# Optimization experiments

Hardware: AMD Instinct MI355X
Metric: run time of the kernel (lower is better)

## Reference

```python
import jax, jax.numpy as jnp
import numpy as np

B, S, H = 2, 2048, 2048
NH, HD = 16, 128
I = 8192
EPS = float(np.finfo(np.float32).eps)  # torch RMSNorm default eps=None -> dtype eps


def rmsnorm(x, w):
    var = jnp.mean(jnp.square(x), axis=-1, keepdims=True)
    return x * jax.lax.rsqrt(var + EPS) * w


def setup_inputs() -> dict:
    key = jax.random.key(0)
    ks = jax.random.split(key, 8)
    s = 0.02
    return {
        "hidden_states": jax.random.normal(ks[0], (B, S, H), jnp.float32),
        "Wq": jax.random.normal(ks[1], (H, H), jnp.float32) * s,
        "Wk": jax.random.normal(ks[2], (H, H), jnp.float32) * s,
        "Wv": jax.random.normal(ks[3], (H, H), jnp.float32) * s,
        "Wo": jax.random.normal(ks[4], (H, H), jnp.float32) * s,
        "Wg": jax.random.normal(ks[5], (I, H), jnp.float32) * s,
        "Wu": jax.random.normal(ks[6], (I, H), jnp.float32) * s,
        "Wd": jax.random.normal(ks[7], (H, I), jnp.float32) * s,
        "g_in": jnp.ones((H,), jnp.float32),
        "g_post": jnp.ones((H,), jnp.float32),
    }


def reference(hidden_states, Wq, Wk, Wv, Wo, Wg, Wu, Wd, g_in, g_post):
    residual = hidden_states
    x = rmsnorm(hidden_states, g_in)
    # projections: nn.Linear does x @ W.T
    q = (x @ Wq.T).reshape(B, S, NH, HD).transpose(0, 2, 1, 3)  # [B,NH,S,HD]
    k = (x @ Wk.T).reshape(B, S, NH, HD).transpose(0, 2, 1, 3)
    v = (x @ Wv.T).reshape(B, S, NH, HD).transpose(0, 2, 1, 3)
    scores = jnp.einsum("bhqd,bhkd->bhqk", q, k) / jnp.sqrt(jnp.float32(HD))
    attn = jax.nn.softmax(scores, axis=-1)
    out = jnp.einsum("bhqk,bhkd->bhqd", attn, v)
    out = out.transpose(0, 2, 1, 3).reshape(B, S, H)
    hidden_states = residual + out @ Wo.T
    residual = hidden_states
    x = rmsnorm(hidden_states, g_post)
    mlp = (jax.nn.silu(x @ Wg.T) * (x @ Wu.T)) @ Wd.T
    return residual + mlp
```

## Files before the change

### kernel.cpp

```cpp
#include <hip/hip_runtime.h>

using u16 = unsigned short;
using u32 = unsigned int;

typedef __attribute__((ext_vector_type(8))) __bf16 bf16x8;
typedef __attribute__((ext_vector_type(4))) float f32x4;

__device__ __forceinline__ u16 f2bf(float f) {
  __bf16 h = (__bf16)f;
  return __builtin_bit_cast(u16, h);
}
__device__ __forceinline__ u32 pk2(float a, float b) {
  return (u32)f2bf(a) | ((u32)f2bf(b) << 16);
}
__device__ __forceinline__ float bf2f(u16 h) {
  return __uint_as_float(((u32)h) << 16);
}
__device__ __forceinline__ void gload16(const u16* g, u16* l) {
  __builtin_amdgcn_global_load_lds((const __attribute__((address_space(1))) void*)g,
                                   (__attribute__((address_space(3))) void*)l, 16, 0, 0);
}
__device__ __forceinline__ f32x4 mfma_bf16(bf16x8 a, bf16x8 b, f32x4 c) {
  return __builtin_amdgcn_mfma_f32_16x16x32_bf16(a, b, c, 0, 0, 0);
}

__global__ __launch_bounds__(256) void cvt_bf16(const float* __restrict__ in,
                                                u16* __restrict__ out, int n8) {
  int i = blockIdx.x * 256 + threadIdx.x;
  int stride = gridDim.x * 256;
  for (; i < n8; i += stride) {
    float4 a = ((const float4*)in)[(size_t)i * 2];
    float4 b = ((const float4*)in)[(size_t)i * 2 + 1];
    ((uint4*)out)[i] = make_uint4(pk2(a.x, a.y), pk2(a.z, a.w), pk2(b.x, b.y), pk2(b.z, b.w));
  }
}

__global__ __launch_bounds__(256) void rmsnorm_bf16(const float* __restrict__ x,
                                                    const float* __restrict__ g,
                                                    u16* __restrict__ o) {
  const int row = blockIdx.x;
  const int tid = threadIdx.x;
  const float4* xr = (const float4*)(x + (size_t)row * 2048);
  float4 a = xr[tid * 2], b = xr[tid * 2 + 1];
  float s = a.x * a.x + a.y * a.y + a.z * a.z + a.w * a.w +
            b.x * b.x + b.y * b.y + b.z * b.z + b.w * b.w;
#pragma unroll
  for (int off = 1; off < 64; off <<= 1) s += __shfl_xor(s, off);
  __shared__ float red[4];
  if ((tid & 63) == 0) red[tid >> 6] = s;
  __syncthreads();
  s = red[0] + red[1] + red[2] + red[3];
  const float r = rsqrtf(s * (1.0f / 2048.0f) + 1.1920929e-07f);
  const float4* gr = (const float4*)g;
  float4 ga = gr[tid * 2], gb = gr[tid * 2 + 1];
  ((uint4*)(o + (size_t)row * 2048))[tid] =
      make_uint4(pk2(a.x * r * ga.x, a.y * r * ga.y), pk2(a.z * r * ga.z, a.w * r * ga.w),
                 pk2(b.x * r * gb.x, b.y * r * gb.y), pk2(b.z * r * gb.z, b.w * r * gb.w));
}

template <int EPI>
__global__ __launch_bounds__(512, 2) void gemm4p(const u16* __restrict__ A,
                                                 const u16* __restrict__ B,
                                                 u16* Cb, float* Cf,
                                                 const float* __restrict__ Res,
                                                 int M, int N, int K, int lda) {
  alignas(16) __shared__ u16 lds[8 * 8192];
  const int tid = threadIdx.x;
  const int w = tid >> 6, lane = tid & 63;
  const int lo = lane & 15, hi = lane >> 4;
  const int nbm = M >> 8, nbx = N >> 8;
  const int RM = nbm >> 1, RN = nbx >> 2;
  const int xcd = blockIdx.x & 7, bidx = blockIdx.x >> 3;
  const int bm = ((xcd >> 2) * RM + bidx / RN) << 8;
  const int bn = ((xcd & 3) * RN + bidx % RN) << 8;
  const int wm = w >> 2, wn = w & 3;

  const int rw = (hi ^ ((lo >> 1) & 3)) * 8;
  const int arow0 = wm * 128 + lo, brow0 = wn * 64 + lo;

  const int srow = tid >> 2;
  const int scol = ((tid & 3) ^ ((tid >> 3) & 3)) * 8;
  const u16* Ab = A + (size_t)(bm + srow) * lda + scol;
  const u16* Bb = B + (size_t)(bn + srow) * K + scol;

  f32x4 acc[8][4] = {};
  bf16x8 af[4], bf[4];

#define SLOT(par, kh, op) ((((par) * 2 + (kh)) * 2 + (op)) * 8192)
#define STG(par, kh, op, kt)                                                   \
  {                                                                            \
    const u16* g_ = (op) ? Bb : Ab;                                            \
    const int ld_ = (op) ? K : lda;                                            \
    gload16(g_ + (kt) + (kh) * 32, &lds[SLOT(par, kh, op) + tid * 8]);         \
    gload16(g_ + (size_t)128 * ld_ + (kt) + (kh) * 32,                         \
            &lds[SLOT(par, kh, op) + 4096 + tid * 8]);                         \
  }
#define PHASE_OPEN()                                       \
  __builtin_amdgcn_s_barrier();                            \
  asm volatile("s_waitcnt lgkmcnt(0)" ::: "memory");       \
  __builtin_amdgcn_sched_barrier(0);
#define MFMA16(mb)                                                             \
  __builtin_amdgcn_s_setprio(1);                                               \
  _Pragma("unroll") for (int m_ = 0; m_ < 4; ++m_)                             \
      _Pragma("unroll") for (int n_ = 0; n_ < 4; ++n_)                         \
          acc[m_ + (mb)][n_] = mfma_bf16(af[m_], bf[n_], acc[m_ + (mb)][n_]);  \
  __builtin_amdgcn_s_setprio(0);

  STG(0, 0, 0, 0); STG(0, 0, 1, 0); STG(0, 1, 0, 0); STG(0, 1, 1, 0);
  asm volatile("s_waitcnt vmcnt(0)" ::: "memory");
  __builtin_amdgcn_s_barrier();

  const int NT = K >> 6;
  for (int t = 0; t < NT; ++t) {
    const int par = t & 1, np = par ^ 1;
    const int ktn = (t + 1) << 6;
    const bool pre = (t + 1 < NT);
    const u16* LA0 = &lds[SLOT(par, 0, 0)];
    const u16* LB0 = &lds[SLOT(par, 0, 1)];
    const u16* LA1 = &lds[SLOT(par, 1, 0)];
    const u16* LB1 = &lds[SLOT(par, 1, 1)];

#pragma unroll
    for (int n = 0; n < 4; ++n) bf[n] = *(const bf16x8*)(LB0 + (brow0 + n * 16) * 32 + rw);
#pragma unroll
    for (int m = 0; m < 4; ++m) af[m] = *(const bf16x8*)(LA0 + (arow0 + m * 16) * 32 + rw);
    if (pre) STG(np, 0, 0, ktn);
    PHASE_OPEN();
    MFMA16(0);
    __builtin_amdgcn_s_barrier();

#pragma unroll
    for (int m = 0; m < 4; ++m)
      af[m] = *(const bf16x8*)(LA0 + (arow0 + (m + 4) * 16) * 32 + rw);
    if (pre) STG(np, 0, 1, ktn);
    PHASE_OPEN();
    MFMA16(4);
    if (pre) { asm volatile("s_waitcnt vmcnt(4)" ::: "memory"); }
    else     { asm volatile("s_waitcnt vmcnt(0)" ::: "memory"); }
    __builtin_amdgcn_s_barrier();

#pragma unroll
    for (int n = 0; n < 4; ++n) bf[n] = *(const bf16x8*)(LB1 + (brow0 + n * 16) * 32 + rw);
#pragma unroll
    for (int m = 0; m < 4; ++m) af[m] = *(const bf16x8*)(LA1 + (arow0 + m * 16) * 32 + rw);
    if (pre) STG(np, 1, 0, ktn);
    PHASE_OPEN();
    MFMA16(0);
    __builtin_amdgcn_s_barrier();

#pragma unroll
    for (int m = 0; m < 4; ++m)
      af[m] = *(const bf16x8*)(LA1 + (arow0 + (m + 4) * 16) * 32 + rw);
    if (pre) STG(np, 1, 1, ktn);
    PHASE_OPEN();
    MFMA16(4);
    if (pre) { asm volatile("s_waitcnt vmcnt(4)" ::: "memory"); }
    __builtin_amdgcn_s_barrier();
  }
#undef SLOT
#undef STG
#undef PHASE_OPEN
#undef MFMA16

#pragma unroll
  for (int m = 0; m < 8; ++m) {
    const int gr = bm + wm * 128 + m * 16 + hi * 4;
#pragma unroll
    for (int n = 0; n < 4; ++n) {
      const int gc = bn + wn * 64 + n * 16 + lo;
#pragma unroll
      for (int r = 0; r < 4; ++r) {
        const size_t idx = (size_t)(gr + r) * N + gc;
        if constexpr (EPI == 1) {
          Cf[idx] = Res[idx] + acc[m][n][r];
        } else if constexpr (EPI == 2) {
          float g = bf2f(Cb[idx]);
          float s = g / (1.f + __expf(-g));
          Cb[idx] = f2bf(s * acc[m][n][r]);
        } else {
          Cb[idx] = f2bf(acc[m][n][r]);
        }
      }
    }
  }
}

template <int EPI>
__global__ __launch_bounds__(512, 1) void gemm3b(const u16* __restrict__ A,
                                                 const u16* __restrict__ B,
                                                 u16* Cb, float* Cf,
                                                 const float* __restrict__ Res,
                                                 int M, int N, int K, int lda) {
  constexpr int BUF = 24576;
  alignas(16) __shared__ u16 lds[3 * BUF];
  const int tid = threadIdx.x;
  const int w = tid >> 6, lane = tid & 63;
  const int lo = lane & 15, hi = lane >> 4;

  const int nbm = M >> 8, nbx = N >> 7;
  const int RM = nbm >> 1, RN = nbx >> 2;
  const int xcd = blockIdx.x & 7, idx = blockIdx.x >> 3;
  const int bm = ((xcd >> 2) * RM + idx / RN) << 8;
  const int bn = ((xcd & 3) * RN + idx % RN) << 7;

  const int wm = w >> 1, wn = w & 1;
  const int scol = ((tid & 7) ^ ((tid >> 3) & 7)) * 8;
  const u16* Ag = A + (size_t)(bm + (tid >> 3)) * lda + scol;
  const u16* Bg = B + (size_t)(bn + (tid >> 3)) * K + scol;

  f32x4 acc[4][4] = {};

#define STG(b, kt)                                                                    \
  {                                                                                   \
    _Pragma("unroll") for (int c = 0; c < 4; ++c)                                     \
        gload16(Ag + (size_t)(c * 64) * lda + (kt), &lds[(b)*BUF + c * 4096 + tid * 8]); \
    _Pragma("unroll") for (int c = 0; c < 2; ++c)                                     \
        gload16(Bg + (size_t)(c * 64) * K + (kt), &lds[(b)*BUF + 16384 + c * 4096 + tid * 8]); \
  }

  const int NT = K >> 6;
  STG(0, 0);
  STG(1, 64);

  int cur = 0;
  for (int T = 0; T < NT; ++T) {
    if (T + 1 < NT) {
      asm volatile("s_waitcnt vmcnt(6)" ::: "memory");
    } else {
      asm volatile("s_waitcnt vmcnt(0)" ::: "memory");
    }
    __builtin_amdgcn_s_barrier();
    __builtin_amdgcn_sched_barrier(0);

    const u16* LA = &lds[cur * BUF];
    const u16* LB = LA + 16384;
    bf16x8 af[4][2], bf[4][2];
#pragma unroll
    for (int ks = 0; ks < 2; ++ks) {
#pragma unroll
      for (int m = 0; m < 4; ++m)
        af[m][ks] = *(const bf16x8*)(LA + (wm * 64 + m * 16 + lo) * 64 +
                                     ((ks * 4 + hi) ^ (lo & 7)) * 8);
#pragma unroll
      for (int n = 0; n < 4; ++n)
        bf[n][ks] = *(const bf16x8*)(LB + (wn * 64 + n * 16 + lo) * 64 +
                                     ((ks * 4 + hi) ^ (lo & 7)) * 8);
    }
    if (T + 2 < NT) {
      const int nb = (cur + 2) % 3;
      STG(nb, (T + 2) << 6);
    }
    __builtin_amdgcn_s_setprio(1);
#pragma unroll
    for (int ks = 0; ks < 2; ++ks)
#pragma unroll
      for (int m = 0; m < 4; ++m)
#pragma unroll
        for (int n = 0; n < 4; ++n) acc[m][n] = mfma_bf16(af[m][ks], bf[n][ks], acc[m][n]);
    __builtin_amdgcn_s_setprio(0);
    cur = (cur + 1) % 3;
  }
#undef STG

#pragma unroll
  for (int m = 0; m < 4; ++m) {
    const int gr = bm + wm * 64 + m * 16 + hi * 4;
#pragma unroll
    for (int n = 0; n < 4; ++n) {
      const int gc = bn + wn * 64 + n * 16 + lo;
#pragma unroll
      for (int r = 0; r < 4; ++r) {
        const size_t idx2 = (size_t)(gr + r) * N + gc;
        if constexpr (EPI == 1) {
          Cf[idx2] = Res[idx2] + acc[m][n][r];
        } else if constexpr (EPI == 2) {
          float g = bf2f(Cb[idx2]);
          float s = g / (1.f + __expf(-g));
          Cb[idx2] = f2bf(s * acc[m][n][r]);
        } else {
          Cb[idx2] = f2bf(acc[m][n][r]);
        }
      }
    }
  }
}

template <int EPI>
__global__ __launch_bounds__(256) void gemm_bt(const u16* __restrict__ A,
                                               const float* __restrict__ B,
                                               u16* Cb, float* Cf, const float* Res,
                                               int M, int N, int K) {
  alignas(16) __shared__ u16 As[128 * 32];
  alignas(16) __shared__ u16 Bs[128 * 32];
  const int tid = threadIdx.x;
  const int w = tid >> 6, lane = tid & 63;
  const int lo = lane & 15, hi = lane >> 4;
  const int bm = blockIdx.y * 128, bn = blockIdx.x * 128;
  const int wr = (w >> 1) * 64, wc = (w & 1) * 64;
  f32x4 acc[4][4] = {};
  const int r0 = tid >> 2, kc0 = (tid & 3) * 8;
  const u16* a0 = A + (size_t)(bm + r0) * K + kc0;
  const u16* a1 = A + (size_t)(bm + 64 + r0) * K + kc0;
  const float* b0 = B + (size_t)(bn + r0) * K + kc0;
  const float* b1 = B + (size_t)(bn + 64 + r0) * K + kc0;
  u16* asd0 = &As[(size_t)tid * 8];
  u16* asd1 = &As[(size_t)(tid + 256) * 8];
  u16* bsd0 = &Bs[(size_t)tid * 8];
  u16* bsd1 = &Bs[(size_t)(tid + 256) * 8];
  for (int kt = 0; kt < K; kt += 32) {
    gload16(a0 + kt, asd0);
    gload16(a1 + kt, asd1);
    float4 x0 = *(const float4*)(b0 + kt);
    float4 x1 = *(const float4*)(b0 + kt + 4);
    float4 y0 = *(const float4*)(b1 + kt);
    float4 y1 = *(const float4*)(b1 + kt + 4);
    *(uint4*)bsd0 = make_uint4(pk2(x0.x, x0.y), pk2(x0.z, x0.w), pk2(x1.x, x1.y), pk2(x1.z, x1.w));
    *(uint4*)bsd1 = make_uint4(pk2(y0.x, y0.y), pk2(y0.z, y0.w), pk2(y1.x, y1.y), pk2(y1.z, y1.w));
    __syncthreads();
    bf16x8 af[4], bfr[4];
#pragma unroll
    for (int i = 0; i < 4; ++i) {
      af[i] = *(const bf16x8*)(&As[(wr + i * 16 + lo) * 32 + hi * 8]);
      bfr[i] = *(const bf16x8*)(&Bs[(wc + i * 16 + lo) * 32 + hi * 8]);
    }
#pragma unroll
    for (int i = 0; i < 4; ++i)
#pragma unroll
      for (int j = 0; j < 4; ++j) acc[i][j] = mfma_bf16(af[i], bfr[j], acc[i][j]);
    __syncthreads();
  }
#pragma unroll
  for (int i = 0; i < 4; ++i) {
    const int gr = bm + wr + i * 16 + hi * 4;
#pragma unroll
    for (int j = 0; j < 4; ++j) {
      const int gc = bn + wc + j * 16 + lo;
#pragma unroll
      for (int r = 0; r < 4; ++r) {
        const size_t idx = (size_t)(gr + r) * N + gc;
        if constexpr (EPI == 1) {
          Cf[idx] = Res[idx] + acc[i][j][r];
        } else if constexpr (EPI == 2) {
          float g = bf2f(Cb[idx]);
          float s = g / (1.f + __expf(-g));
          Cb[idx] = f2bf(s * acc[i][j][r]);
        } else {
          Cb[idx] = f2bf(acc[i][j][r]);
        }
      }
    }
  }
}

__global__ __launch_bounds__(256) void transpose_v(const u16* __restrict__ v,
                                                   u16* __restrict__ vt, int ldv) {
  __shared__ u16 t[32][33];
  const int bh = blockIdx.z, b = bh >> 4, h = bh & 15;
  const int s0 = blockIdx.x * 32, d0 = blockIdx.y * 32;
  const int tx = threadIdx.x, ty = threadIdx.y;
#pragma unroll
  for (int i = 0; i < 4; ++i)
    t[ty + i * 8][tx] = v[(size_t)(b * 2048 + s0 + ty + i * 8) * ldv + h * 128 + d0 + tx];
  __syncthreads();
#pragma unroll
  for (int i = 0; i < 4; ++i)
    vt[(size_t)(bh * 128 + d0 + ty + i * 8) * 2048 + s0 + tx] = t[tx][ty + i * 8];
}

__global__ __launch_bounds__(256) void attn_fwd2(const u16* __restrict__ q,
                                                 const u16* __restrict__ k,
                                                 const u16* __restrict__ vt,
                                                 u16* o, int ldq) {
  constexpr int S = 2048;
  alignas(16) __shared__ u16 Ks[2][64 * 128];
  alignas(16) __shared__ u16 Vs[2][128 * 64];
  alignas(16) __shared__ u16 plds[4][16 * 68];
  const int bh = blockIdx.y, b = bh >> 4, h = bh & 15;
  const int tid = threadIdx.x, w = tid >> 6, lane = tid & 63;
  const int lo = lane & 15, hi = lane >> 4;
  const int qr = blockIdx.x * 64 + w * 16;
  u16* pl = &plds[w][0];

  bf16x8 qf[4];
  const u16* qb = q + (size_t)(b * S + qr + lo) * ldq + h * 128 + hi * 8;
#pragma unroll
  for (int ks = 0; ks < 4; ++ks) qf[ks] = *(const bf16x8*)(qb + ks * 32);

  f32x4 oacc[8] = {};
  f32x4 lp = {0.f, 0.f, 0.f, 0.f};

  const u16* kb = k + (size_t)(b * S) * ldq + h * 128;
  const u16* vb = vt + (size_t)bh * 128 * S;

  const int kcs = ((((tid & 15) * 16) ^ (((tid >> 4) & 7) << 4)) >> 1);
  const int vcs = ((((tid & 7) * 16) ^ (((tid >> 3) & 7) << 4)) >> 1);
  const u16* kgs = kb + (size_t)(tid >> 4) * ldq + kcs;
  const u16* vgs = vb + (size_t)(tid >> 3) * S + vcs;

  int cur = 0;
#pragma unroll
  for (int c = 0; c < 4; ++c) gload16(kgs + (size_t)(c * 16) * ldq, &Ks[0][c * 2048 + tid * 8]);
#pragma unroll
  for (int c = 0; c < 4; ++c) gload16(vgs + (size_t)(c * 32) * S, &Vs[0][c * 2048 + tid * 8]);
  __syncthreads();

  const int swq = (lo & 7) << 4;
  constexpr float SCL = 0.12752956f;

  for (int kv = 0; kv < S; kv += 64) {
    if (kv + 64 < S) {
      const int nb = cur ^ 1;
#pragma unroll
      for (int c = 0; c < 4; ++c)
        gload16(kgs + (size_t)(kv + 64 + c * 16) * ldq, &Ks[nb][c * 2048 + tid * 8]);
#pragma unroll
      for (int c = 0; c < 4; ++c)
        gload16(vgs + (size_t)(c * 32) * S + kv + 64, &Vs[nb][c * 2048 + tid * 8]);
    }
    const u16* Kc = &Ks[cur][0];
    const u16* Vc = &Vs[cur][0];

    f32x4 sacc[4] = {};
    __builtin_amdgcn_s_setprio(1);
#pragma unroll
    for (int ks = 0; ks < 4; ++ks)
#pragma unroll
      for (int n = 0; n < 4; ++n) {
        bf16x8 kf = *(const bf16x8*)(Kc + (n * 16 + lo) * 128 + (((ks * 64 + hi * 16) ^ swq) >> 1));
        sacc[n] = mfma_bf16(qf[ks], kf, sacc[n]);
      }
    __builtin_amdgcn_s_setprio(0);

    f32x4 p[4];
#pragma unroll
    for (int n = 0; n < 4; ++n)
#pragma unroll
      for (int r = 0; r < 4; ++r) p[n][r] = exp2f(sacc[n][r] * SCL);
#pragma unroll
    for (int r = 0; r < 4; ++r)
      lp[r] += (p[0][r] + p[1][r]) + (p[2][r] + p[3][r]);

#pragma unroll
    for (int n = 0; n < 4; ++n)
#pragma unroll
      for (int r = 0; r < 4; ++r)
        pl[(hi * 4 + r) * 68 + n * 16 + lo] = f2bf(p[n][r]);
    asm volatile("s_waitcnt lgkmcnt(0)" ::: "memory");
    bf16x8 pf0 = *(const bf16x8*)(pl + lo * 68 + hi * 8);
    bf16x8 pf1 = *(const bf16x8*)(pl + lo * 68 + 32 + hi * 8);

    __builtin_amdgcn_s_setprio(1);
#pragma unroll
    for (int f = 0; f < 8; ++f) {
      const int row = f * 16 + lo;
      bf16x8 vf0 = *(const bf16x8*)(Vc + row * 64 + (((hi * 16) ^ swq) >> 1));
      bf16x8 vf1 = *(const bf16x8*)(Vc + row * 64 + (((64 + hi * 16) ^ swq) >> 1));
      oacc[f] = mfma_bf16(pf0, vf0, oacc[f]);
      oacc[f] = mfma_bf16(pf1, vf1, oacc[f]);
    }
    __builtin_amdgcn_s_setprio(0);

    __syncthreads();
    cur ^= 1;
  }

  float l[4];
#pragma unroll
  for (int r = 0; r < 4; ++r) l[r] = lp[r];
#pragma unroll
  for (int off = 1; off < 16; off <<= 1)
#pragma unroll
    for (int r = 0; r < 4; ++r) l[r] += __shfl_xor(l[r], off);

  u16* ob = o + (size_t)(b * S + qr) * ldq + h * 128;
#pragma unroll
  for (int f = 0; f < 8; ++f)
#pragma unroll
    for (int r = 0; r < 4; ++r)
      ob[(size_t)(hi * 4 + r) * ldq + f * 16 + lo] = f2bf(oacc[f][r] / l[r]);
}

extern "C" void kernel_launch(void* const* d_in, const int* in_sizes, int n_in,
                              void* d_out, int out_size, void* d_ws, size_t ws_size,
                              hipStream_t stream) {
  constexpr int B = 2, S = 2048, H = 2048, NH = 16, I = 8192;
  constexpr int M = B * S;

  const float* hs = (const float*)d_in[0];
  const float* Wq = (const float*)d_in[1];
  const float* Wk = (const float*)d_in[2];
  const float* Wv = (const float*)d_in[3];
  const float* Wo = (const float*)d_in[4];
  const float* Wg = (const float*)d_in[5];
  const float* Wu = (const float*)d_in[6];
  const float* Wd = (const float*)d_in[7];
  const float* g_in = (const float*)d_in[8];
  const float* g_post = (const float*)d_in[9];
  float* out = (float*)d_out;

  constexpr size_t SZ_HH = (size_t)H * H * 2;
  constexpr size_t SZ_IH = (size_t)I * H * 2;
  constexpr size_t SZ_MH = (size_t)M * H * 2;
  constexpr size_t NEED_NEW = SZ_MH + 3 * SZ_MH + SZ_MH + SZ_IH;

  if (ws_size >= NEED_NEW) {
    char* p = (char*)d_ws;
    u16* x_b = (u16*)p;    p += SZ_MH;
    u16* qkv_b = (u16*)p;  p += 3 * SZ_MH;
    u16* vt_b = (u16*)p;   p += SZ_MH;
    u16* wsc = (u16*)p;    p += SZ_IH;
    u16* gate_b = qkv_b;

    rmsnorm_bf16<<<M, 256, 0, stream>>>(hs, g_in, x_b);

    cvt_bf16<<<1024, 256, 0, stream>>>(Wq, wsc, H * H / 8);
    cvt_bf16<<<1024, 256, 0, stream>>>(Wk, wsc + (size_t)H * H, H * H / 8);
    cvt_bf16<<<1024, 256, 0, stream>>>(Wv, wsc + (size_t)2 * H * H, H * H / 8);
    gemm4p<0><<<(M / 256) * (3 * H / 256), 512, 0, stream>>>(
        x_b, wsc, qkv_b, nullptr, nullptr, M, 3 * H, H, H);

    transpose_v<<<dim3(S / 32, 128 / 32, B * NH), dim3(32, 8), 0, stream>>>(
        qkv_b + 2 * H, vt_b, 3 * H);
    attn_fwd2<<<dim3(S / 64, B * NH), 256, 0, stream>>>(qkv_b, qkv_b + H, vt_b, qkv_b, 3 * H);

    cvt_bf16<<<1024, 256, 0, stream>>>(Wo, wsc, H * H / 8);
    gemm3b<1><<<(M / 256) * (H / 128), 512, 0, stream>>>(
        qkv_b, wsc, nullptr, out, hs, M, H, H, 3 * H);

    rmsnorm_bf16<<<M, 256, 0, stream>>>(out, g_post, x_b);

    cvt_bf16<<<1024, 256, 0, stream>>>(Wg, wsc, I * H / 8);
    gemm4p<0><<<(M / 256) * (I / 256), 512, 0, stream>>>(
        x_b, wsc, gate_b, nullptr, nullptr, M, I, H, H);
    cvt_bf16<<<1024, 256, 0, stream>>>(Wu, wsc, I * H / 8);
    gemm4p<2><<<(M / 256) * (I / 256), 512, 0, stream>>>(
        x_b, wsc, gate_b, nullptr, nullptr, M, I, H, H);
    cvt_bf16<<<1024, 256, 0, stream>>>(Wd, wsc, I * H / 8);
    gemm3b<1><<<(M / 256) * (H / 128), 512, 0, stream>>>(
        gate_b, wsc, nullptr, out, out, M, H, I, I);
    return;
  }

  constexpr int MC = 2048;
  char* p = (char*)d_ws;
  u16* x_b = (u16*)p;   p += SZ_MH;
  u16* q_b = (u16*)p;   p += SZ_MH;
  u16* k_b = (u16*)p;   p += SZ_MH;
  u16* v_b = (u16*)p;   p += SZ_MH;
  u16* vt_b = (u16*)p;  p += SZ_MH;
  u16* g_mlp = k_b;

  rmsnorm_bf16<<<M, 256, 0, stream>>>(hs, g_in, x_b);
  const dim3 gHH(H / 128, M / 128);
  gemm_bt<0><<<gHH, 256, 0, stream>>>(x_b, Wq, q_b, nullptr, nullptr, M, H, H);
  gemm_bt<0><<<gHH, 256, 0, stream>>>(x_b, Wk, k_b, nullptr, nullptr, M, H, H);
  gemm_bt<0><<<gHH, 256, 0, stream>>>(x_b, Wv, v_b, nullptr, nullptr, M, H, H);
  transpose_v<<<dim3(S / 32, 128 / 32, B * NH), dim3(32, 8), 0, stream>>>(v_b, vt_b, H);
  attn_fwd2<<<dim3(S / 64, B * NH), 256, 0, stream>>>(q_b, k_b, vt_b, q_b, H);
  gemm_bt<1><<<gHH, 256, 0, stream>>>(q_b, Wo, nullptr, out, hs, M, H, H);
  rmsnorm_bf16<<<M, 256, 0, stream>>>(out, g_post, x_b);
  const dim3 gIH(I / 128, MC / 128), gHI(H / 128, MC / 128);
  for (int mc = 0; mc < M / MC; ++mc) {
    const u16* xc = x_b + (size_t)mc * MC * H;
    float* oc = out + (size_t)mc * MC * H;
    gemm_bt<0><<<gIH, 256, 0, stream>>>(xc, Wg, g_mlp, nullptr, nullptr, MC, I, H);
    gemm_bt<2><<<gIH, 256, 0, stream>>>(xc, Wu, g_mlp, nullptr, nullptr, MC, I, H);
    gemm_bt<1><<<gHI, 256, 0, stream>>>(g_mlp, Wd, nullptr, oc, oc, MC, H, I);
  }
}
```

Measured before the change: 859.6 us.

## Fuse gate and up GEMMs, widen attention blocks, use gemm3b for QKV

```diff
diff --git a/kernel.cpp b/kernel.cpp
--- a/kernel.cpp
+++ b/kernel.cpp
@@ -58,55 +58,60 @@
                  pk2(b.x * r * gb.x, b.y * r * gb.y), pk2(b.z * r * gb.z, b.w * r * gb.w));
 }
 
-template <int EPI>
-__global__ __launch_bounds__(512, 2) void gemm4p(const u16* __restrict__ A,
-                                                 const u16* __restrict__ B,
-                                                 u16* Cb, float* Cf,
-                                                 const float* __restrict__ Res,
-                                                 int M, int N, int K, int lda) {
-  alignas(16) __shared__ u16 lds[8 * 8192];
+__global__ __launch_bounds__(512, 2) void gemmGU(const u16* __restrict__ A,
+                                                 const u16* __restrict__ Bg,
+                                                 const u16* __restrict__ Bu,
+                                                 u16* __restrict__ Out,
+                                                 int M, int N, int K) {
+  alignas(16) __shared__ u16 lds[2 * 32768];
   const int tid = threadIdx.x;
   const int w = tid >> 6, lane = tid & 63;
   const int lo = lane & 15, hi = lane >> 4;
-  const int nbm = M >> 8, nbx = N >> 8;
+  const int nbm = M >> 8, nbx = N >> 7;
   const int RM = nbm >> 1, RN = nbx >> 2;
   const int xcd = blockIdx.x & 7, bidx = blockIdx.x >> 3;
   const int bm = ((xcd >> 2) * RM + bidx / RN) << 8;
-  const int bn = ((xcd & 3) * RN + bidx % RN) << 8;
-  const int wm = w >> 2, wn = w & 3;
+  const int bn = ((xcd & 3) * RN + bidx % RN) << 7;
+  const int wm = w >> 1, wn = w & 1;
 
   const int rw = (hi ^ ((lo >> 1) & 3)) * 8;
-  const int arow0 = wm * 128 + lo, brow0 = wn * 64 + lo;
+  const int arow0 = wm * 64 + lo, brow0 = wn * 64 + lo;
 
   const int srow = tid >> 2;
   const int scol = ((tid & 3) ^ ((tid >> 3) & 3)) * 8;
-  const u16* Ab = A + (size_t)(bm + srow) * lda + scol;
-  const u16* Bb = B + (size_t)(bn + srow) * K + scol;
-
-  f32x4 acc[8][4] = {};
+  const u16* Ab = A + (size_t)(bm + srow) * K + scol;
+  const u16* Bgb = Bg + (size_t)(bn + srow) * K + scol;
+  const u16* Bub = Bu + (size_t)(bn + srow) * K + scol;
+
+  f32x4 gacc[4][4] = {}, uacc[4][4] = {};
   bf16x8 af[4], bf[4];
 
-#define SLOT(par, kh, op) ((((par) * 2 + (kh)) * 2 + (op)) * 8192)
-#define STG(par, kh, op, kt)                                                   \
-  {                                                                            \
-    const u16* g_ = (op) ? Bb : Ab;                                            \
-    const int ld_ = (op) ? K : lda;                                            \
-    gload16(g_ + (kt) + (kh) * 32, &lds[SLOT(par, kh, op) + tid * 8]);         \
-    gload16(g_ + (size_t)128 * ld_ + (kt) + (kh) * 32,                         \
-            &lds[SLOT(par, kh, op) + 4096 + tid * 8]);                         \
-  }
-#define PHASE_OPEN()                                       \
-  __builtin_amdgcn_s_barrier();                            \
-  asm volatile("s_waitcnt lgkmcnt(0)" ::: "memory");       \
+#define AOFF(par, kh) ((par)*32768 + (kh)*8192)
+#define BGOFF(par, kh) ((par)*32768 + 16384 + (kh)*4096)
+#define BUOFF(par, kh) ((par)*32768 + 24576 + (kh)*4096)
+#define STG_A(par, kh, kt)                                                  \
+  {                                                                         \
+    gload16(Ab + (kt) + (kh)*32, &lds[AOFF(par, kh) + tid * 8]);            \
+    gload16(Ab + (size_t)128 * K + (kt) + (kh)*32,                          \
+            &lds[AOFF(par, kh) + 4096 + tid * 8]);                          \
+  }
+#define STG_B(par, kh, kt)                                                  \
+  {                                                                         \
+    gload16(Bgb + (kt) + (kh)*32, &lds[BGOFF(par, kh) + tid * 8]);          \
+    gload16(Bub + (kt) + (kh)*32, &lds[BUOFF(par, kh) + tid * 8]);          \
+  }
+#define PHASE_OPEN()                                   \
+  __builtin_amdgcn_s_barrier();                        \
+  asm volatile("s_waitcnt lgkmcnt(0)" ::: "memory");   \
   __builtin_amdgcn_sched_barrier(0);
-#define MFMA16(mb)                                                             \
-  __builtin_amdgcn_s_setprio(1);                                               \
-  _Pragma("unroll") for (int m_ = 0; m_ < 4; ++m_)                             \
-      _Pragma("unroll") for (int n_ = 0; n_ < 4; ++n_)                         \
-          acc[m_ + (mb)][n_] = mfma_bf16(af[m_], bf[n_], acc[m_ + (mb)][n_]);  \
+#define MFMA16(ACC)                                                         \
+  __builtin_amdgcn_s_setprio(1);                                            \
+  _Pragma("unroll") for (int m_ = 0; m_ < 4; ++m_)                          \
+      _Pragma("unroll") for (int n_ = 0; n_ < 4; ++n_)                      \
+          ACC[m_][n_] = mfma_bf16(af[m_], bf[n_], ACC[m_][n_]);             \
   __builtin_amdgcn_s_setprio(0);
 
-  STG(0, 0, 0, 0); STG(0, 0, 1, 0); STG(0, 1, 0, 0); STG(0, 1, 1, 0);
+  STG_A(0, 0, 0); STG_B(0, 0, 0); STG_A(0, 1, 0); STG_B(0, 1, 0);
   asm volatile("s_waitcnt vmcnt(0)" ::: "memory");
   __builtin_amdgcn_s_barrier();
 
@@ -115,71 +120,67 @@
     const int par = t & 1, np = par ^ 1;
     const int ktn = (t + 1) << 6;
     const bool pre = (t + 1 < NT);
-    const u16* LA0 = &lds[SLOT(par, 0, 0)];
-    const u16* LB0 = &lds[SLOT(par, 0, 1)];
-    const u16* LA1 = &lds[SLOT(par, 1, 0)];
-    const u16* LB1 = &lds[SLOT(par, 1, 1)];
-
-#pragma unroll
-    for (int n = 0; n < 4; ++n) bf[n] = *(const bf16x8*)(LB0 + (brow0 + n * 16) * 32 + rw);
-#pragma unroll
-    for (int m = 0; m < 4; ++m) af[m] = *(const bf16x8*)(LA0 + (arow0 + m * 16) * 32 + rw);
-    if (pre) STG(np, 0, 0, ktn);
+
+#pragma unroll
+    for (int n = 0; n < 4; ++n)
+      bf[n] = *(const bf16x8*)(&lds[BGOFF(par, 0)] + (brow0 + n * 16) * 32 + rw);
+#pragma unroll
+    for (int m = 0; m < 4; ++m)
+      af[m] = *(const bf16x8*)(&lds[AOFF(par, 0)] + (arow0 + m * 16) * 32 + rw);
+    if (pre) STG_A(np, 0, ktn);
     PHASE_OPEN();
-    MFMA16(0);
+    MFMA16(gacc);
     __builtin_amdgcn_s_barrier();
 
 #pragma unroll
-    for (int m = 0; m < 4; ++m)
-      af[m] = *(const bf16x8*)(LA0 + (arow0 + (m + 4) * 16) * 32 + rw);
-    if (pre) STG(np, 0, 1, ktn);
+    for (int n = 0; n < 4; ++n)
+      bf[n] = *(const bf16x8*)(&lds[BUOFF(par, 0)] + (brow0 + n * 16) * 32 + rw);
+    if (pre) STG_B(np, 0, ktn);
     PHASE_OPEN();
-    MFMA16(4);
+    MFMA16(uacc);
     if (pre) { asm volatile("s_waitcnt vmcnt(4)" ::: "memory"); }
     else     { asm volatile("s_waitcnt vmcnt(0)" ::: "memory"); }
     __builtin_amdgcn_s_barrier();
 
 #pragma unroll
-    for (int n = 0; n < 4; ++n) bf[n] = *(const bf16x8*)(LB1 + (brow0 + n * 16) * 32 + rw);
-#pragma unroll
-    for (int m = 0; m < 4; ++m) af[m] = *(const bf16x8*)(LA1 + (arow0 + m * 16) * 32 + rw);
-    if (pre) STG(np, 1, 0, ktn);
+    for (int n = 0; n < 4; ++n)
+      bf[n] = *(const bf16x8*)(&lds[BGOFF(par, 1)] + (brow0 + n * 16) * 32 + rw);
+#pragma unroll
+    for (int m = 0; m < 4; ++m)
+      af[m] = *(const bf16x8*)(&lds[AOFF(par, 1)] + (arow0 + m * 16) * 32 + rw);
+    if (pre) STG_A(np, 1, ktn);
     PHASE_OPEN();
-    MFMA16(0);
+    MFMA16(gacc);
     __builtin_amdgcn_s_barrier();
 
 #pragma unroll
-    for (int m = 0; m < 4; ++m)
-      af[m] = *(const bf16x8*)(LA1 + (arow0 + (m + 4) * 16) * 32 + rw);
-    if (pre) STG(np, 1, 1, ktn);
+    for (int n = 0; n < 4; ++n)
+      bf[n] = *(const bf16x8*)(&lds[BUOFF(par, 1)] + (brow0 + n * 16) * 32 + rw);
+    if (pre) STG_B(np, 1, ktn);
     PHASE_OPEN();
-    MFMA16(4);
+    MFMA16(uacc);
     if (pre) { asm volatile("s_waitcnt vmcnt(4)" ::: "memory"); }
     __builtin_amdgcn_s_barrier();
   }
-#undef SLOT
-#undef STG
+#undef AOFF
+#undef BGOFF
+#undef BUOFF
+#undef STG_A
+#undef STG_B
 #undef PHASE_OPEN
 #undef MFMA16
 
 #pragma unroll
-  for (int m = 0; m < 8; ++m) {
-    const int gr = bm + wm * 128 + m * 16 + hi * 4;
+  for (int m = 0; m < 4; ++m) {
+    const int gr = bm + wm * 64 + m * 16 + hi * 4;
 #pragma unroll
     for (int n = 0; n < 4; ++n) {
       const int gc = bn + wn * 64 + n * 16 + lo;
 #pragma unroll
       for (int r = 0; r < 4; ++r) {
-        const size_t idx = (size_t)(gr + r) * N + gc;
-        if constexpr (EPI == 1) {
-          Cf[idx] = Res[idx] + acc[m][n][r];
-        } else if constexpr (EPI == 2) {
-          float g = bf2f(Cb[idx]);
-          float s = g / (1.f + __expf(-g));
-          Cb[idx] = f2bf(s * acc[m][n][r]);
-        } else {
-          Cb[idx] = f2bf(acc[m][n][r]);
-        }
+        float g = gacc[m][n][r];
+        float s = g / (1.f + __expf(-g));
+        Out[(size_t)(gr + r) * N + gc] = f2bf(s * uacc[m][n][r]);
       }
     }
   }
@@ -367,18 +368,18 @@
     vt[(size_t)(bh * 128 + d0 + ty + i * 8) * 2048 + s0 + tx] = t[tx][ty + i * 8];
 }
 
-__global__ __launch_bounds__(256) void attn_fwd2(const u16* __restrict__ q,
+__global__ __launch_bounds__(512) void attn_fwd3(const u16* __restrict__ q,
                                                  const u16* __restrict__ k,
                                                  const u16* __restrict__ vt,
                                                  u16* o, int ldq) {
   constexpr int S = 2048;
   alignas(16) __shared__ u16 Ks[2][64 * 128];
   alignas(16) __shared__ u16 Vs[2][128 * 64];
-  alignas(16) __shared__ u16 plds[4][16 * 68];
+  alignas(16) __shared__ u16 plds[8][16 * 68];
   const int bh = blockIdx.y, b = bh >> 4, h = bh & 15;
   const int tid = threadIdx.x, w = tid >> 6, lane = tid & 63;
   const int lo = lane & 15, hi = lane >> 4;
-  const int qr = blockIdx.x * 64 + w * 16;
+  const int qr = blockIdx.x * 128 + w * 16;
   u16* pl = &plds[w][0];
 
   bf16x8 qf[4];
@@ -392,16 +393,16 @@
   const u16* kb = k + (size_t)(b * S) * ldq + h * 128;
   const u16* vb = vt + (size_t)bh * 128 * S;
 
-  const int kcs = ((((tid & 15) * 16) ^ (((tid >> 4) & 7) << 4)) >> 1);
-  const int vcs = ((((tid & 7) * 16) ^ (((tid >> 3) & 7) << 4)) >> 1);
+  const int kcs = ((tid & 15) ^ ((tid >> 4) & 7)) * 8;
+  const int vcs = ((tid & 7) ^ ((tid >> 3) & 7)) * 8;
   const u16* kgs = kb + (size_t)(tid >> 4) * ldq + kcs;
   const u16* vgs = vb + (size_t)(tid >> 3) * S + vcs;
 
   int cur = 0;
 #pragma unroll
-  for (int c = 0; c < 4; ++c) gload16(kgs + (size_t)(c * 16) * ldq, &Ks[0][c * 2048 + tid * 8]);
-#pragma unroll
-  for (int c = 0; c < 4; ++c) gload16(vgs + (size_t)(c * 32) * S, &Vs[0][c * 2048 + tid * 8]);
+  for (int c = 0; c < 2; ++c) gload16(kgs + (size_t)(c * 32) * ldq, &Ks[0][c * 4096 + tid * 8]);
+#pragma unroll
+  for (int c = 0; c < 2; ++c) gload16(vgs + (size_t)(c * 64) * S, &Vs[0][c * 4096 + tid * 8]);
   __syncthreads();
 
   const int swq = (lo & 7) << 4;
@@ -411,11 +412,11 @@
     if (kv + 64 < S) {
       const int nb = cur ^ 1;
 #pragma unroll
-      for (int c = 0; c < 4; ++c)
-        gload16(kgs + (size_t)(kv + 64 + c * 16) * ldq, &Ks[nb][c * 2048 + tid * 8]);
-#pragma unroll
-      for (int c = 0; c < 4; ++c)
-        gload16(vgs + (size_t)(c * 32) * S + kv + 64, &Vs[nb][c * 2048 + tid * 8]);
+      for (int c = 0; c < 2; ++c)
+        gload16(kgs + (size_t)(kv + 64 + c * 32) * ldq, &Ks[nb][c * 4096 + tid * 8]);
+#pragma unroll
+      for (int c = 0; c < 2; ++c)
+        gload16(vgs + (size_t)(c * 64) * S + kv + 64, &Vs[nb][c * 4096 + tid * 8]);
     }
     const u16* Kc = &Ks[cur][0];
     const u16* Vc = &Vs[cur][0];
@@ -501,27 +502,30 @@
   constexpr size_t SZ_HH = (size_t)H * H * 2;
   constexpr size_t SZ_IH = (size_t)I * H * 2;
   constexpr size_t SZ_MH = (size_t)M * H * 2;
-  constexpr size_t NEED_NEW = SZ_MH + 3 * SZ_MH + SZ_MH + SZ_IH;
-
-  if (ws_size >= NEED_NEW) {
+  constexpr size_t NEED_BASE = SZ_MH + 3 * SZ_MH + SZ_MH + SZ_IH;
+  constexpr size_t NEED_FUSED = NEED_BASE + SZ_IH;
+
+  if (ws_size >= NEED_BASE) {
     char* p = (char*)d_ws;
     u16* x_b = (u16*)p;    p += SZ_MH;
     u16* qkv_b = (u16*)p;  p += 3 * SZ_MH;
     u16* vt_b = (u16*)p;   p += SZ_MH;
     u16* wsc = (u16*)p;    p += SZ_IH;
     u16* gate_b = qkv_b;
+    const bool fused = ws_size >= NEED_FUSED;
+    u16* wu_b = fused ? (u16*)p : nullptr;
 
     rmsnorm_bf16<<<M, 256, 0, stream>>>(hs, g_in, x_b);
 
     cvt_bf16<<<1024, 256, 0, stream>>>(Wq, wsc, H * H / 8);
     cvt_bf16<<<1024, 256, 0, stream>>>(Wk, wsc + (size_t)H * H, H * H / 8);
     cvt_bf16<<<1024, 256, 0, stream>>>(Wv, wsc + (size_t)2 * H * H, H * H / 8);
-    gemm4p<0><<<(M / 256) * (3 * H / 256), 512, 0, stream>>>(
+    gemm3b<0><<<(M / 256) * (3 * H / 128), 512, 0, stream>>>(
         x_b, wsc, qkv_b, nullptr, nullptr, M, 3 * H, H, H);
 
     transpose_v<<<dim3(S / 32, 128 / 32, B * NH), dim3(32, 8), 0, stream>>>(
         qkv_b + 2 * H, vt_b, 3 * H);
-    attn_fwd2<<<dim3(S / 64, B * NH), 256, 0, stream>>>(qkv_b, qkv_b + H, vt_b, qkv_b, 3 * H);
+    attn_fwd3<<<dim3(S / 128, B * NH), 512, 0, stream>>>(qkv_b, qkv_b + H, vt_b, qkv_b, 3 * H);
 
     cvt_bf16<<<1024, 256, 0, stream>>>(Wo, wsc, H * H / 8);
     gemm3b<1><<<(M / 256) * (H / 128), 512, 0, stream>>>(
@@ -529,12 +533,18 @@
 
     rmsnorm_bf16<<<M, 256, 0, stream>>>(out, g_post, x_b);
 
-    cvt_bf16<<<1024, 256, 0, stream>>>(Wg, wsc, I * H / 8);
-    gemm4p<0><<<(M / 256) * (I / 256), 512, 0, stream>>>(
-        x_b, wsc, gate_b, nullptr, nullptr, M, I, H, H);
-    cvt_bf16<<<1024, 256, 0, stream>>>(Wu, wsc, I * H / 8);
-    gemm4p<2><<<(M / 256) * (I / 256), 512, 0, stream>>>(
-        x_b, wsc, gate_b, nullptr, nullptr, M, I, H, H);
+    if (fused) {
+      cvt_bf16<<<1024, 256, 0, stream>>>(Wg, wsc, I * H / 8);
+      cvt_bf16<<<1024, 256, 0, stream>>>(Wu, wu_b, I * H / 8);
+      gemmGU<<<(M / 256) * (I / 128), 512, 0, stream>>>(x_b, wsc, wu_b, gate_b, M, I, H);
+    } else {
+      cvt_bf16<<<1024, 256, 0, stream>>>(Wg, wsc, I * H / 8);
+      gemm3b<0><<<(M / 256) * (I / 128), 512, 0, stream>>>(
+          x_b, wsc, gate_b, nullptr, nullptr, M, I, H, H);
+      cvt_bf16<<<1024, 256, 0, stream>>>(Wu, wsc, I * H / 8);
+      gemm3b<2><<<(M / 256) * (I / 128), 512, 0, stream>>>(
+          x_b, wsc, gate_b, nullptr, nullptr, M, I, H, H);
+    }
     cvt_bf16<<<1024, 256, 0, stream>>>(Wd, wsc, I * H / 8);
     gemm3b<1><<<(M / 256) * (H / 128), 512, 0, stream>>>(
         gate_b, wsc, nullptr, out, out, M, H, I, I);
@@ -556,7 +566,7 @@
   gemm_bt<0><<<gHH, 256, 0, stream>>>(x_b, Wk, k_b, nullptr, nullptr, M, H, H);
   gemm_bt<0><<<gHH, 256, 0, stream>>>(x_b, Wv, v_b, nullptr, nullptr, M, H, H);
   transpose_v<<<dim3(S / 32, 128 / 32, B * NH), dim3(32, 8), 0, stream>>>(v_b, vt_b, H);
-  attn_fwd2<<<dim3(S / 64, B * NH), 256, 0, stream>>>(q_b, k_b, vt_b, q_b, H);
+  attn_fwd3<<<dim3(S / 128, B * NH), 512, 0, stream>>>(q_b, k_b, vt_b, q_b, H);
   gemm_bt<1><<<gHH, 256, 0, stream>>>(q_b, Wo, nullptr, out, hs, M, H, H);
   rmsnorm_bf16<<<M, 256, 0, stream>>>(out, g_post, x_b);
   const dim3 gIH(I / 128, MC / 128), gHI(H / 128, MC / 128);
```

Result: faster. 779.1 us (-9.4%).
